# Kernel optimization log

Measured on AMD Instinct MI355X. Metric: run time of the kernel, lower is better.

The kernel has to match this reference:

```python
import jax, jax.numpy as jnp
import numpy as np

D_MODEL = 1024
N_HEADS = 16
HEAD_DIM = D_MODEL // N_HEADS


def setup_inputs() -> dict:
    key = jax.random.key(0)
    k1, k2, k3 = jax.random.split(key, 3)
    x = jax.random.normal(k1, (2, 2048, D_MODEL), dtype=jnp.float32)
    w_qkv = jax.random.normal(k2, (3 * D_MODEL, D_MODEL), dtype=jnp.float32) * 0.02
    w_out = jax.random.normal(k3, (D_MODEL, D_MODEL), dtype=jnp.float32) * 0.02
    return {"x": x, "w_qkv": w_qkv, "w_out": w_out}


def reference(x, w_qkv, w_out):
    B, T, D = x.shape
    H, Hd = N_HEADS, HEAD_DIM
    # QKV projection: Linear stores weight as [out, in] -> '...i,oi->...o'
    qkv = jnp.einsum('bti,oi->bto', x, w_qkv)              # [B, T, 3D]
    # split (3*H, Hs) group-major, chunk into q/k/v of H heads each
    qkv = qkv.reshape(B, T, 3, H, Hd)
    q = jnp.transpose(qkv[:, :, 0], (0, 2, 1, 3))          # [B, H, T, Hd]
    k = jnp.transpose(qkv[:, :, 1], (0, 2, 1, 3))
    v = jnp.transpose(qkv[:, :, 2], (0, 2, 1, 3))
    scale = 1.0 / jnp.sqrt(jnp.asarray(Hd, dtype=x.dtype))
    scores = jnp.einsum('bhqd,bhkd->bhqk', q, k) * scale   # [B, H, T, T]
    causal = jnp.tril(jnp.ones((T, T), dtype=bool))        # [T, T]
    scores = jnp.where(causal[None, None], scores, jnp.asarray(-jnp.inf, dtype=scores.dtype))
    attn = jax.nn.softmax(scores, axis=-1)
    ctx = jnp.einsum('bhqk,bhkd->bhqd', attn, v)           # [B, H, T, Hd]
    ctx = jnp.transpose(ctx, (0, 2, 1, 3)).reshape(B, T, D)
    return jnp.einsum('bti,oi->bto', ctx, w_out)
```

## Files before the change

### kernel.cpp

```cpp
#include <hip/hip_runtime.h>


typedef short short8 __attribute__((ext_vector_type(8)));
typedef float f32x4 __attribute__((ext_vector_type(4)));
typedef unsigned short u16;
typedef unsigned int u32;

#define T_SEQ 2048
#define N_B 2
#define N_H 16
#define HD 64
#define DM 1024
#define TRIPLE 3072

__device__ __forceinline__ u16 f2bf(float f) {
  union { float f; unsigned u; } v;
  v.f = f;
  unsigned r = v.u + 0x7fffu + ((v.u >> 16) & 1u);
  return (u16)(r >> 16);
}

__device__ __forceinline__ float bf2f(u16 x) {
  return __uint_as_float((u32)x << 16);
}

__device__ __forceinline__ u32 cvtpk(float a, float b) {
  u32 r;
  asm("v_cvt_pk_bf16_f32 %0, %1, %2" : "=v"(r) : "v"(a), "v"(b));
  return r;
}

typedef const __attribute__((address_space(1))) void gvoid;
typedef __attribute__((address_space(3))) void lvoid;

__device__ __forceinline__ void g2l16(const void* g, void* l) {
  __builtin_amdgcn_global_load_lds((gvoid*)g, (lvoid*)l, 16, 0, 0);
}

__device__ __forceinline__ void storeC(float* p, float v) { *p = v; }
__device__ __forceinline__ void storeC(u16* p, float v) { *p = f2bf(v); }

__global__ __launch_bounds__(256) void cast_all(const float4* __restrict__ x,
                                                const float4* __restrict__ wq,
                                                const float4* __restrict__ wo,
                                                ushort4* __restrict__ out) {
  int i = blockIdx.x * 256 + threadIdx.x;
  const float4* src;
  int off;
  if (i < 1048576) { src = x; off = 0; }
  else if (i < 1835008) { src = wq; off = 1048576; }
  else { src = wo; off = 1835008; }
  float4 v = src[i - off];
  ushort4 o;
  o.x = f2bf(v.x); o.y = f2bf(v.y); o.z = f2bf(v.z); o.w = f2bf(v.w);
  out[i] = o;
}

__global__ __launch_bounds__(256) void vtrans(const u16* __restrict__ qkv,
                                              u16* __restrict__ vT) {
  const int tid = threadIdx.x;
  const int w = tid >> 6, lane = tid & 63;
  const int ti = lane >> 3, di = lane & 7;
  const int h = blockIdx.y, b = blockIdx.z;
  const int t0 = blockIdx.x * 256 + w * 64 + ti * 8;

  const u16* src = qkv + (size_t)(b * T_SEQ + t0) * TRIPLE + 2 * DM + h * HD + di * 8;
  u32 x[8][4];
#pragma unroll
  for (int e = 0; e < 8; ++e) {
    union { short8 v; u32 u[4]; } cv;
    cv.v = *(const short8*)(src + (size_t)e * TRIPLE);
#pragma unroll
    for (int j = 0; j < 4; ++j) x[e][j] = cv.u[j];
  }
  u32 y[8][4];
#pragma unroll
  for (int a = 0; a < 4; ++a)
#pragma unroll
    for (int j = 0; j < 4; ++j) {
      u32 lo = x[2 * a][j], hi = x[2 * a + 1][j];
      y[2 * a][j] = (lo & 0x0000FFFFu) | (hi << 16);
      y[2 * a + 1][j] = (lo >> 16) | (hi & 0xFFFF0000u);
    }
  u16* dst = vT + ((size_t)(b * N_H + h) * HD + di * 8) * T_SEQ + t0;
#pragma unroll
  for (int dd = 0; dd < 8; ++dd) {
    union { short8 v; u32 u[4]; } cv;
#pragma unroll
    for (int a = 0; a < 4; ++a) cv.u[a] = y[2 * a + (dd & 1)][dd >> 1];
    *(short8*)(dst + (size_t)dd * T_SEQ) = cv.v;
  }
}

template <typename OutT>
__global__ __launch_bounds__(256) void gemm_bt(const u16* __restrict__ A,
                                               const u16* __restrict__ W,
                                               OutT* __restrict__ C,
                                               int M, int N, int K) {
  __shared__ char As[128 * 64 * 2];
  __shared__ char Bs[128 * 64 * 2];
  const int tid = threadIdx.x;
  const int lane = tid & 63, w = tid >> 6;
  const int l15 = lane & 15, l4 = lane >> 4;
  const int m0 = blockIdx.y * 128, n0 = blockIdx.x * 128;
  const int wr = (w >> 1) * 64, wc = (w & 1) * 64;

  const f32x4 zero = {0.f, 0.f, 0.f, 0.f};
  f32x4 acc[4][4];
#pragma unroll
  for (int m = 0; m < 4; ++m)
#pragma unroll
    for (int n = 0; n < 4; ++n) acc[m][n] = zero;

  for (int k0 = 0; k0 < K; k0 += 64) {
#pragma unroll
    for (int i = 0; i < 4; ++i) {
      const int cb = (i * 4 + w) * 64;
      const int c = cb + lane;
      const int row = c >> 3;
      const int ks = ((c & 7) ^ (row & 7)) * 8;
      g2l16(A + (size_t)(m0 + row) * K + k0 + ks, As + (size_t)cb * 16);
      g2l16(W + (size_t)(n0 + row) * K + k0 + ks, Bs + (size_t)cb * 16);
    }
    __syncthreads();

#pragma unroll
    for (int kk = 0; kk < 2; ++kk) {
      short8 a[4], b[4];
#pragma unroll
      for (int m = 0; m < 4; ++m) {
        int row = wr + m * 16 + l15;
        int slot = (kk * 4 + l4) ^ (row & 7);
        a[m] = *(const short8*)(As + row * 128 + slot * 16);
      }
#pragma unroll
      for (int n = 0; n < 4; ++n) {
        int row = wc + n * 16 + l15;
        int slot = (kk * 4 + l4) ^ (row & 7);
        b[n] = *(const short8*)(Bs + row * 128 + slot * 16);
      }
#pragma unroll
      for (int m = 0; m < 4; ++m)
#pragma unroll
        for (int n = 0; n < 4; ++n)
          acc[m][n] = __builtin_amdgcn_mfma_f32_16x16x32_bf16(a[m], b[n], acc[m][n], 0, 0, 0);
    }
    __syncthreads();
  }

#pragma unroll
  for (int m = 0; m < 4; ++m)
#pragma unroll
    for (int n = 0; n < 4; ++n)
#pragma unroll
      for (int r = 0; r < 4; ++r) {
        int row = m0 + wr + m * 16 + l4 * 4 + r;
        int col = n0 + wc + n * 16 + l15;
        storeC(C + (size_t)row * N + col, acc[m][n][r]);
      }
}

__global__ __launch_bounds__(512) void attn_fwd(const u16* __restrict__ qkv,
                                                const u16* __restrict__ vT,
                                                u16* __restrict__ ctx) {
  __shared__ char Ks[3][8192];
  __shared__ char Vs[3][8192];
  __shared__ char Pl[8][2048];

  const int tid = threadIdx.x;
  const int lane = tid & 63, w = tid >> 6;
  const int l15 = lane & 15, l4 = lane >> 4;
  const int g = blockIdx.x;
  const int p = blockIdx.y;
  const int h = g & 15, b = g >> 4;
  const int q0A = 128 * p, q0B = 128 * (15 - p);
  const int nA = 2 * p + 2;

  const float c_log2 = 0.18033688011112042f;
  short8 qa2[2][2];
#pragma unroll
  for (int ps = 0; ps < 2; ++ps) {
    const int qq0 = ps ? q0B : q0A;
    const u16* qp = qkv + (size_t)(b * T_SEQ + qq0 + w * 16 + l15) * TRIPLE + h * HD;
#pragma unroll
    for (int kk = 0; kk < 2; ++kk) {
      short8 raw = *(const short8*)(qp + kk * 32 + l4 * 8);
      union { short8 v; u32 w4[4]; } qq;
#pragma unroll
      for (int j = 0; j < 4; ++j)
        qq.w4[j] = cvtpk(bf2f((u16)raw[2 * j]) * c_log2,
                         bf2f((u16)raw[2 * j + 1]) * c_log2);
      qa2[ps][kk] = qq.v;
    }
  }

  const int r0 = tid >> 3, c0 = tid & 7;
  const int swz = (c0 ^ (r0 & 7)) << 3;
  const u16* kbase = qkv + (size_t)(b * T_SEQ + r0) * TRIPLE + DM + h * HD + swz;
  const u16* vbase = vT + ((size_t)g * HD + r0) * T_SEQ + swz;

#define STAGE(kt_, buf_)                                                     \
  {                                                                          \
    g2l16(kbase + (size_t)((kt_) * (64 * TRIPLE)), Ks[buf_] + tid * 16);     \
    g2l16(vbase + (u32)((kt_) * 64), Vs[buf_] + tid * 16);                   \
  }

  char* Plb = Pl[w];

  const f32x4 zero = {0.f, 0.f, 0.f, 0.f};
  f32x4 o[4];
#pragma unroll
  for (int nt = 0; nt < 4; ++nt) o[nt] = zero;
  float mr = -INFINITY, lr = 0.f;
  short8 qa0 = qa2[0][0], qa1 = qa2[0][1];
  int q0 = q0A;

  STAGE(0, 0);
  STAGE(1, 1);
  asm volatile("s_waitcnt vmcnt(2)\n\ts_barrier" ::: "memory");

  int cur = 0;
  for (int i = 0;; ++i) {
    const int kt = (i < nA) ? i : 33 - i;

    if (i + 2 < 34) {
      const int kt2 = (i + 2 < nA) ? (i + 2) : 31 - i;
      int sb = cur - 1;
      if (sb < 0) sb = 2;
      STAGE(kt2, sb);
    }

    const int k0 = kt * 64;
    if (k0 <= q0 + w * 16) {
      f32x4 s[4];
#pragma unroll
      for (int mt = 0; mt < 4; ++mt) s[mt] = zero;
      __builtin_amdgcn_s_setprio(1);
#pragma unroll
      for (int mt = 0; mt < 4; ++mt) {
        int row = mt * 16 + l15;
        int slot0 = l4 ^ (row & 7);
        short8 kb0 = *(const short8*)(Ks[cur] + row * 128 + slot0 * 16);
        s[mt] = __builtin_amdgcn_mfma_f32_16x16x32_bf16(kb0, qa0, s[mt], 0, 0, 0);
        int slot1 = (4 + l4) ^ (row & 7);
        short8 kb1 = *(const short8*)(Ks[cur] + row * 128 + slot1 * 16);
        s[mt] = __builtin_amdgcn_mfma_f32_16x16x32_bf16(kb1, qa1, s[mt], 0, 0, 0);
      }
      __builtin_amdgcn_s_setprio(0);

      if (i >= nA - 2 && i <= nA + 1) {
        const int qrow = q0 + w * 16 + l15;
#pragma unroll
        for (int mt = 0; mt < 4; ++mt)
#pragma unroll
          for (int r = 0; r < 4; ++r) {
            int key = k0 + mt * 16 + l4 * 4 + r;
            if (key > qrow) s[mt][r] = -INFINITY;
          }
      }

      float mx = fmaxf(fmaxf(fmaxf(s[0][0], s[0][1]), fmaxf(s[0][2], s[0][3])),
                       fmaxf(fmaxf(s[1][0], s[1][1]), fmaxf(s[1][2], s[1][3])));
      mx = fmaxf(mx, fmaxf(fmaxf(fmaxf(s[2][0], s[2][1]), fmaxf(s[2][2], s[2][3])),
                           fmaxf(fmaxf(s[3][0], s[3][1]), fmaxf(s[3][2], s[3][3]))));
      mx = fmaxf(mx, __shfl_xor(mx, 16));
      mx = fmaxf(mx, __shfl_xor(mx, 32));
      if (!__all(mx - mr <= 8.0f)) {
        float mn = fmaxf(mr, mx);
        float fr = exp2f(mr - mn);
        lr *= fr;
#pragma unroll
        for (int r = 0; r < 4; ++r) {
          float frq = __shfl(fr, l4 * 4 + r);
#pragma unroll
          for (int nt = 0; nt < 4; ++nt) o[nt][r] *= frq;
        }
        mr = mn;
      }
      float ps = 0.f;
#pragma unroll
      for (int mt = 0; mt < 4; ++mt)
#pragma unroll
        for (int r = 0; r < 4; ++r) {
          float pv = exp2f(s[mt][r] - mr);
          s[mt][r] = pv;
          ps += pv;
        }
      lr += ps;

#pragma unroll
      for (int mt = 0; mt < 4; ++mt) {
        uint2 pw;
        pw.x = cvtpk(s[mt][0], s[mt][1]);
        pw.y = cvtpk(s[mt][2], s[mt][3]);
        int slot = ((mt * 2 + (l4 >> 1)) ^ (l15 & 7));
        *(uint2*)(Plb + l15 * 128 + (slot << 4) + ((l4 & 1) << 3)) = pw;
      }

      __builtin_amdgcn_s_setprio(1);
#pragma unroll
      for (int kk = 0; kk < 2; ++kk) {
        short8 pa = *(const short8*)(Plb + l15 * 128 + (((kk * 4 + l4) ^ (l15 & 7)) << 4));
#pragma unroll
        for (int nt = 0; nt < 4; ++nt) {
          int d = nt * 16 + l15;
          int slot = (kk * 4 + l4) ^ (l15 & 7);
          short8 vb = *(const short8*)(Vs[cur] + d * 128 + slot * 16);
          o[nt] = __builtin_amdgcn_mfma_f32_16x16x32_bf16(pa, vb, o[nt], 0, 0, 0);
        }
      }
      __builtin_amdgcn_s_setprio(0);
    }

    if (i == nA - 1 || i == 33) {
      lr += __shfl_xor(lr, 16);
      lr += __shfl_xor(lr, 32);
#pragma unroll
      for (int r = 0; r < 4; ++r) {
        float lrq = __shfl(lr, l4 * 4 + r);
        float inv = __builtin_amdgcn_rcpf(lrq);
        size_t t = (size_t)(b * T_SEQ + q0 + w * 16 + l4 * 4 + r);
#pragma unroll
        for (int nt = 0; nt < 4; ++nt)
          ctx[t * DM + h * HD + nt * 16 + l15] = f2bf(o[nt][r] * inv);
      }
      if (i == 33) break;
#pragma unroll
      for (int nt = 0; nt < 4; ++nt) o[nt] = zero;
      mr = -INFINITY; lr = 0.f;
      qa0 = qa2[1][0]; qa1 = qa2[1][1];
      q0 = q0B;
    }

    if (i == 32)
      asm volatile("s_waitcnt vmcnt(0)\n\ts_barrier" ::: "memory");
    else
      asm volatile("s_waitcnt vmcnt(2)\n\ts_barrier" ::: "memory");
    cur = (cur == 2) ? 0 : cur + 1;
  }
#undef STAGE
}

extern "C" void kernel_launch(void* const* d_in, const int* in_sizes, int n_in,
                              void* d_out, int out_size, void* d_ws, size_t ws_size,
                              hipStream_t stream) {
  const float* x = (const float*)d_in[0];
  const float* wqkv = (const float*)d_in[1];
  const float* wout = (const float*)d_in[2];
  float* out = (float*)d_out;
  char* ws = (char*)d_ws;

  u16* xb    = (u16*)(ws);
  u16* wqkvb = (u16*)(ws + 8u * 1024 * 1024);
  u16* woutb = (u16*)(ws + 14u * 1024 * 1024);
  u16* qkvb  = (u16*)(ws + 16u * 1024 * 1024);
  u16* ctxb  = (u16*)(ws + 40u * 1024 * 1024);
  u16* vTb   = (u16*)(ws + 48u * 1024 * 1024);

  cast_all<<<8192, 256, 0, stream>>>((const float4*)x, (const float4*)wqkv,
                                     (const float4*)wout, (ushort4*)xb);

  gemm_bt<u16><<<dim3(24, 32), 256, 0, stream>>>(xb, wqkvb, qkvb, 4096, 3072, 1024);

  vtrans<<<dim3(8, N_H, N_B), 256, 0, stream>>>(qkvb, vTb);

  attn_fwd<<<dim3(32, 8), 512, 0, stream>>>(qkvb, vTb, ctxb);

  gemm_bt<float><<<dim3(8, 32), 256, 0, stream>>>(ctxb, woutb, out, 4096, 1024, 1024);
}
```

Measured before the change: 126.9 us.

## Use 256x256 double-buffered GEMM tile for QKV projection

Adds a new GEMM kernel with 256x256 output tiles, 512 threads (8 waves) and double-buffered LDS staging with swizzled layout, and uses it for the QKV projection. Larger tiles raise arithmetic intensity and cut global loads per FLOP, and double buffering overlaps the next k-tile's loads with MFMA work. The cost is 128 KB of LDS per block, which may limit occupancy, and only 192 blocks for 256 CUs, so some CUs sit idle.

Measured after the change: 129.9 us. +2.4%, slower.

```diff
diff --git a/kernel.cpp b/kernel.cpp
--- a/kernel.cpp
+++ b/kernel.cpp
@@ -93,6 +93,100 @@
 }
 
 template <typename OutT>
+__global__ __launch_bounds__(512, 2) void gemm_bt_256(const u16* __restrict__ A,
+                                                      const u16* __restrict__ W,
+                                                      OutT* __restrict__ C,
+                                                      int M, int N, int K) {
+  __shared__ char As[2][32768];
+  __shared__ char Bs[2][32768];
+
+  const int tid = threadIdx.x;
+  const int lane = tid & 63, w = tid >> 6;
+  const int l15 = lane & 15, l4 = lane >> 4;
+  const int wm = w >> 2, wn = w & 3;
+  const int m0 = blockIdx.y * 256, n0 = blockIdx.x * 256;
+
+  const int srow = tid >> 3;
+  const int sswz = ((tid & 7) ^ (srow & 7)) << 3;
+  const u16* Abase = A + (size_t)(m0 + srow) * K + sswz;
+  const u16* Bbase = W + (size_t)(n0 + srow) * K + sswz;
+
+  const f32x4 zero = {0.f, 0.f, 0.f, 0.f};
+  f32x4 acc[8][4];
+#pragma unroll
+  for (int am = 0; am < 8; ++am)
+#pragma unroll
+    for (int n = 0; n < 4; ++n) acc[am][n] = zero;
+
+#define STAGE8(k0_, buf_)                                                      \
+  {                                                                            \
+    _Pragma("unroll") for (int r_ = 0; r_ < 4; ++r_) {                         \
+      g2l16(Abase + (size_t)(64 * r_) * K + (k0_),                             \
+            As[buf_] + (r_ * 512 + tid) * 16);                                 \
+      g2l16(Bbase + (size_t)(64 * r_) * K + (k0_),                             \
+            Bs[buf_] + (r_ * 512 + tid) * 16);                                 \
+    }                                                                          \
+  }
+
+  STAGE8(0, 0);
+
+  const int nkt = K >> 6;
+  for (int kt = 0;; ++kt) {
+    const int cur = kt & 1;
+
+    if (kt + 1 < nkt) {
+      STAGE8((kt + 1) << 6, cur ^ 1);
+      asm volatile("s_waitcnt vmcnt(8)" ::: "memory");
+    } else {
+      asm volatile("s_waitcnt vmcnt(0)" ::: "memory");
+    }
+    __builtin_amdgcn_s_barrier();
+
+#pragma unroll
+    for (int ph = 0; ph < 4; ++ph) {
+      const int kk = ph >> 1, mh = ph & 1;
+      short8 a[4], b[4];
+#pragma unroll
+      for (int m = 0; m < 4; ++m) {
+        int row = wm * 128 + mh * 64 + m * 16 + l15;
+        int slot = (kk * 4 + l4) ^ (row & 7);
+        a[m] = *(const short8*)(As[cur] + row * 128 + slot * 16);
+      }
+#pragma unroll
+      for (int n = 0; n < 4; ++n) {
+        int row = wn * 64 + n * 16 + l15;
+        int slot = (kk * 4 + l4) ^ (row & 7);
+        b[n] = *(const short8*)(Bs[cur] + row * 128 + slot * 16);
+      }
+      asm volatile("s_waitcnt lgkmcnt(0)" ::: "memory");
+      __builtin_amdgcn_s_setprio(1);
+#pragma unroll
+      for (int m = 0; m < 4; ++m)
+#pragma unroll
+        for (int n = 0; n < 4; ++n)
+          acc[mh * 4 + m][n] =
+              __builtin_amdgcn_mfma_f32_16x16x32_bf16(a[m], b[n], acc[mh * 4 + m][n], 0, 0, 0);
+      __builtin_amdgcn_s_setprio(0);
+    }
+
+    if (kt + 1 >= nkt) break;
+    __builtin_amdgcn_s_barrier();
+  }
+#undef STAGE8
+
+#pragma unroll
+  for (int am = 0; am < 8; ++am)
+#pragma unroll
+    for (int n = 0; n < 4; ++n)
+#pragma unroll
+      for (int r = 0; r < 4; ++r) {
+        int row = m0 + wm * 128 + (am >> 2) * 64 + (am & 3) * 16 + l4 * 4 + r;
+        int col = n0 + wn * 64 + n * 16 + l15;
+        storeC(C + (size_t)row * N + col, acc[am][n][r]);
+      }
+}
+
+template <typename OutT>
 __global__ __launch_bounds__(256) void gemm_bt(const u16* __restrict__ A,
                                                const u16* __restrict__ W,
                                                OutT* __restrict__ C,
@@ -360,7 +454,7 @@
   cast_all<<<8192, 256, 0, stream>>>((const float4*)x, (const float4*)wqkv,
                                      (const float4*)wout, (ushort4*)xb);
 
-  gemm_bt<u16><<<dim3(24, 32), 256, 0, stream>>>(xb, wqkvb, qkvb, 4096, 3072, 1024);
+  gemm_bt_256<u16><<<dim3(12, 16), 512, 0, stream>>>(xb, wqkvb, qkvb, 4096, 3072, 1024);
 
   vtrans<<<dim3(8, N_H, N_B), 256, 0, stream>>>(qkvb, vTb);
 
```
